# Kernel tuning notes

Measured on AMD Instinct MI355X. Metric: run time of the kernel, lower is better.

The kernel has to match this reference:

```python
import jax, jax.numpy as jnp
import numpy as np

B, N, G, K = 4, 8192, 512, 32          # batch, points, num_group, group_size
D, H, DEPTH, ENC, MLP = 768, 12, 4, 256, 3072
HD = D // H


def _fps(xyz, npoint):
    """Farthest point sampling, starts at index 0 (as pointnet2_utils). xyz: [B,N,3] -> idx [B,npoint]."""
    b, n, _ = xyz.shape
    def step(carry, _):
        dmin, far = carry                                   # dmin [b,n], far [b]
        c = jax.vmap(lambda p, i: p[i])(xyz, far)           # [b,3]
        d = jnp.sum((xyz - c[:, None, :]) ** 2, -1)         # [b,n]
        dmin = jnp.minimum(dmin, d)
        nxt = jnp.argmax(dmin, -1).astype(jnp.int32)
        return (dmin, nxt), far
    init = (jnp.full((b, n), 1e10, jnp.float32), jnp.zeros((b,), jnp.int32))
    _, idx = jax.lax.scan(step, init, None, length=npoint)
    return jnp.transpose(idx)                                # [b, npoint]


def _sqdist(a, b):
    # [B,S,C] x [B,M,C] -> [B,S,M] squared euclidean
    return (jnp.sum(a * a, -1)[:, :, None]
            - 2.0 * jnp.einsum('bsc,bmc->bsm', a, b)
            + jnp.sum(b * b, -1)[:, None, :])


def _bn(x, g, b, m, v):   # eval-mode BatchNorm1d, channels-last
    return (x - m) * jax.lax.rsqrt(v + 1e-5) * g + b


def _ln(x, g, b):
    mu = jnp.mean(x, -1, keepdims=True)
    va = jnp.var(x, -1, keepdims=True)
    return (x - mu) * jax.lax.rsqrt(va + 1e-5) * g + b


def setup_inputs():
    key = jax.random.key(0)
    cnt = [0]
    def rn(shape, s=0.02):
        cnt[0] += 1
        return jax.random.normal(jax.random.fold_in(key, cnt[0]), shape, jnp.float32) * s
    inp = dict(
        pts=jax.random.uniform(jax.random.fold_in(key, 1000), (B, N, 3), jnp.float32),
        colors=jax.random.uniform(jax.random.fold_in(key, 1001), (B, N, 3), jnp.float32),
        enc_w1a=rn((128, 6), 0.2), enc_b1a=rn((128,)),
        bn1_g=jnp.ones((128,)), bn1_b=jnp.zeros((128,)), bn1_m=jnp.zeros((128,)), bn1_v=jnp.ones((128,)),
        enc_w1b=rn((256, 128), 0.05), enc_b1b=rn((256,)),
        enc_w2a=rn((512, 512), 0.03), enc_b2a=rn((512,)),
        bn2_g=jnp.ones((512,)), bn2_b=jnp.zeros((512,)), bn2_m=jnp.zeros((512,)), bn2_v=jnp.ones((512,)),
        enc_w2b=rn((ENC, 512), 0.03), enc_b2b=rn((ENC,)),
        e2t_w=rn((D, ENC), 0.04), e2t_b=rn((D,)),
        cls_token=jnp.zeros((1, 1, D)), cls_pos=rn((1, 1, D), 1.0),
        pe_w1=rn((128, 3), 0.3), pe_b1=rn((128,)),
        pe_w2=rn((D, 128), 0.05), pe_b2=rn((D,)),
        ln1_g=jnp.ones((DEPTH, D)), ln1_b=jnp.zeros((DEPTH, D)),
        qkv_w=rn((DEPTH, D, 3 * D)), qkv_b=rn((DEPTH, 3 * D)),
        proj_w=rn((DEPTH, D, D)), proj_b=rn((DEPTH, D)),
        ln2_g=jnp.ones((DEPTH, D)), ln2_b=jnp.zeros((DEPTH, D)),
        mlp_w1=rn((DEPTH, D, MLP)), mlp_b1=rn((DEPTH, MLP)),
        mlp_w2=rn((DEPTH, MLP, D)), mlp_b2=rn((DEPTH, D)),
        fcn_g=jnp.ones((D,)), fcn_b=jnp.zeros((D,)),
        t2e_w=rn((D, D)), t2e_b=rn((D,)),
    )
    return inp


def reference(pts, colors, enc_w1a, enc_b1a, bn1_g, bn1_b, bn1_m, bn1_v,
              enc_w1b, enc_b1b, enc_w2a, enc_b2a, bn2_g, bn2_b, bn2_m, bn2_v,
              enc_w2b, enc_b2b, e2t_w, e2t_b, cls_token, cls_pos,
              pe_w1, pe_b1, pe_w2, pe_b2,
              ln1_g, ln1_b, qkv_w, qkv_b, proj_w, proj_b,
              ln2_g, ln2_b, mlp_w1, mlp_b1, mlp_w2, mlp_b2,
              fcn_g, fcn_b, t2e_w, t2e_b):
    b = pts.shape[0]
    # ---- Group: FPS centers + kNN grouping ----
    fidx = _fps(pts, G)                                        # [B,G]
    center = jax.vmap(lambda p, i: p[i])(pts, fidx)            # [B,G,3]
    d = _sqdist(center, pts)                                   # [B,G,N]
    _, knn = jax.lax.top_k(-d, K)                              # [B,G,K] smallest dists
    nbr = jax.vmap(lambda p, i: p[i])(pts, knn)                # [B,G,K,3]
    nbr_c = jax.vmap(lambda p, i: p[i])(colors, knn)           # [B,G,K,3]
    nbr = nbr - center[:, :, None, :]
    feat = jnp.concatenate([nbr, nbr_c], -1)                   # [B,G,K,6]
    # ---- mini-PointNet Encoder (conv1d k=1 == linear over channels) ----
    x = feat.reshape(b * G, K, 6)
    f = jax.nn.relu(_bn(x @ enc_w1a.T + enc_b1a, bn1_g, bn1_b, bn1_m, bn1_v))
    f = f @ enc_w1b.T + enc_b1b                                # [M,K,256]
    fg = jnp.max(f, axis=1, keepdims=True)                     # [M,1,256]
    f = jnp.concatenate([jnp.broadcast_to(fg, (b * G, K, 256)), f], -1)  # [M,K,512]
    f = jax.nn.relu(_bn(f @ enc_w2a.T + enc_b2a, bn2_g, bn2_b, bn2_m, bn2_v))
    f = f @ enc_w2b.T + enc_b2b                                # [M,K,ENC]
    tok = jnp.max(f, axis=1).reshape(b, G, ENC)                # [B,G,ENC]
    # ---- to transformer ----
    tok = tok @ e2t_w.T + e2t_b                                # [B,G,D]
    pos = jax.nn.gelu(center @ pe_w1.T + pe_b1, approximate=False) @ pe_w2.T + pe_b2
    xs = jnp.concatenate([jnp.broadcast_to(cls_token, (b, 1, D)), tok], 1)
    ps = jnp.concatenate([jnp.broadcast_to(cls_pos, (b, 1, D)), pos], 1)
    xs = xs + ps                                               # [B,G+1,D]
    s = G + 1
    scale = HD ** -0.5
    for i in range(DEPTH):
        h = _ln(xs, ln1_g[i], ln1_b[i])
        qkv = (h @ qkv_w[i] + qkv_b[i]).reshape(b, s, 3, H, HD)
        q, k, v = qkv[:, :, 0], qkv[:, :, 1], qkv[:, :, 2]
        att = jax.nn.softmax(jnp.einsum('bshd,bthd->bhst', q, k) * scale, -1)
        o = jnp.einsum('bhst,bthd->bshd', att, v).reshape(b, s, D)
        xs = xs + o @ proj_w[i] + proj_b[i]
        h = _ln(xs, ln2_g[i], ln2_b[i])
        h = jax.nn.gelu(h @ mlp_w1[i] + mlp_b1[i], approximate=False) @ mlp_w2[i] + mlp_b2[i]
        xs = xs + h
    xs = _ln(xs, fcn_g, fcn_b)
    return xs @ t2e_w.T + t2e_b                                # [B,G+1,embed_dim]
```

## Files before the change

### kernel.cpp

```cpp
#include <hip/hip_runtime.h>
#include <math.h>

#define BB 4
#define NN 8192
#define GG 512
#define KK 32
#define DD 768
#define SS 513
#define HH 12

typedef __attribute__((ext_vector_type(8))) short bf16x8;
typedef __attribute__((ext_vector_type(4))) float f32x4;

__device__ __forceinline__ float gelu_f(float x) {
  return 0.5f * x * (1.f + erff(x * 0.70710678118654752f));
}
__device__ __forceinline__ unsigned short f2b(float f) {
  unsigned u = __float_as_uint(f);
  u = (u + 0x7FFFu + ((u >> 16) & 1u)) >> 16;
  return (unsigned short)u;
}
__device__ __forceinline__ float b2f(unsigned short h) {
  return __uint_as_float(((unsigned)h) << 16);
}

__device__ __forceinline__ unsigned wave_max_u32(unsigned v) {
  unsigned t;
  t = (unsigned)__builtin_amdgcn_update_dpp(0, (int)v, 0x111, 0xf, 0xf, false); v = t > v ? t : v;
  t = (unsigned)__builtin_amdgcn_update_dpp(0, (int)v, 0x112, 0xf, 0xf, false); v = t > v ? t : v;
  t = (unsigned)__builtin_amdgcn_update_dpp(0, (int)v, 0x114, 0xf, 0xf, false); v = t > v ? t : v;
  t = (unsigned)__builtin_amdgcn_update_dpp(0, (int)v, 0x118, 0xf, 0xf, false); v = t > v ? t : v;
  t = (unsigned)__builtin_amdgcn_update_dpp(0, (int)v, 0x142, 0xf, 0xf, false); v = t > v ? t : v;
  t = (unsigned)__builtin_amdgcn_update_dpp(0, (int)v, 0x143, 0xf, 0xf, false); v = t > v ? t : v;
  return (unsigned)__builtin_amdgcn_readlane((int)v, 63);
}
__device__ __forceinline__ unsigned wave_min_u32(unsigned v) {
  unsigned t;
  t = (unsigned)__builtin_amdgcn_update_dpp(0x7FFFFFFF, (int)v, 0x111, 0xf, 0xf, false); v = t < v ? t : v;
  t = (unsigned)__builtin_amdgcn_update_dpp(0x7FFFFFFF, (int)v, 0x112, 0xf, 0xf, false); v = t < v ? t : v;
  t = (unsigned)__builtin_amdgcn_update_dpp(0x7FFFFFFF, (int)v, 0x114, 0xf, 0xf, false); v = t < v ? t : v;
  t = (unsigned)__builtin_amdgcn_update_dpp(0x7FFFFFFF, (int)v, 0x118, 0xf, 0xf, false); v = t < v ? t : v;
  t = (unsigned)__builtin_amdgcn_update_dpp(0x7FFFFFFF, (int)v, 0x142, 0xf, 0xf, false); v = t < v ? t : v;
  t = (unsigned)__builtin_amdgcn_update_dpp(0x7FFFFFFF, (int)v, 0x143, 0xf, 0xf, false); v = t < v ? t : v;
  return (unsigned)__builtin_amdgcn_readlane((int)v, 63);
}

__global__ __launch_bounds__(512) void fps_kernel(const float* __restrict__ pts,
                                                  int* __restrict__ fidx,
                                                  float* __restrict__ center) {
  int b = blockIdx.x;
  int tid = threadIdx.x;
  const float* P = pts + (size_t)b * NN * 3;
  float x[16], y[16], z[16], dmin[16];
#pragma unroll
  for (int j = 0; j < 16; j++) {
    int p = tid + 512 * j;
    x[j] = P[p * 3 + 0]; y[j] = P[p * 3 + 1]; z[j] = P[p * 3 + 2];
    dmin[j] = 1e10f;
  }
  __shared__ unsigned long long sbest;
  __shared__ float scx, scy, scz;
  if (tid == 0) {
    sbest = 0ull;
    scx = x[0]; scy = y[0]; scz = z[0];
    fidx[b * GG] = 0;
    center[(size_t)(b * GG) * 3 + 0] = x[0];
    center[(size_t)(b * GG) * 3 + 1] = y[0];
    center[(size_t)(b * GG) * 3 + 2] = z[0];
  }
  __syncthreads();
  for (int it = 0; it < GG - 1; it++) {
    float cx = scx, cy = scy, cz = scz;
    unsigned bv = 0u, bi = 0x7FFFFFFFu;
    int bj = 0;
#pragma unroll
    for (int j = 0; j < 16; j++) {
      float dx = __fsub_rn(x[j], cx);
      float dy = __fsub_rn(y[j], cy);
      float dz = __fsub_rn(z[j], cz);
      float d = __fadd_rn(__fadd_rn(__fmul_rn(dx, dx), __fmul_rn(dy, dy)), __fmul_rn(dz, dz));
      float dm = fminf(dmin[j], d);
      dmin[j] = dm;
      unsigned db = __float_as_uint(dm);
      if (db > bv) { bv = db; bi = (unsigned)(tid + 512 * j); bj = j; }
    }
    unsigned wmax = wave_max_u32(bv);
    unsigned cand = (bv == wmax) ? bi : 0x7FFFFFFFu;
    unsigned widx = wave_min_u32(cand);
    bool wave_winner = (bv == wmax) && (bi == widx);
    unsigned long long mykey = ((unsigned long long)wmax << 32) | (unsigned long long)(0xFFFFFFFFu - widx);
    if (wave_winner) atomicMax(&sbest, mykey);
    __syncthreads();
    if (wave_winner) {
      if (sbest == mykey) {
        scx = x[bj]; scy = y[bj]; scz = z[bj];
        fidx[b * GG + it + 1] = (int)bi;
        center[(size_t)(b * GG + it + 1) * 3 + 0] = x[bj];
        center[(size_t)(b * GG + it + 1) * 3 + 1] = y[bj];
        center[(size_t)(b * GG + it + 1) * 3 + 2] = z[bj];
        sbest = 0ull;
      }
    }
    __syncthreads();
  }
}

__global__ __launch_bounds__(256) void knn_kernel(const float* __restrict__ pts,
                                                  const float* __restrict__ center,
                                                  int* __restrict__ knn_idx) {
  int bg = blockIdx.x;
  int b = bg >> 9;
  int tid = threadIdx.x;
  __shared__ float dist[NN];
  __shared__ unsigned long long sred[4];
  const float* P = pts + (size_t)b * NN * 3;
  float cx = center[bg * 3 + 0], cy = center[bg * 3 + 1], cz = center[bg * 3 + 2];
  for (int j = 0; j < 32; j++) {
    int p = tid + 256 * j;
    float dx = P[p * 3 + 0] - cx, dy = P[p * 3 + 1] - cy, dz = P[p * 3 + 2] - cz;
    dist[p] = dx * dx + dy * dy + dz * dz;
  }
  __syncthreads();
  for (int r = 0; r < KK; r++) {
    unsigned long long best = 0xFFFFFFFFFFFFFFFFull;
#pragma unroll 8
    for (int j = 0; j < 32; j++) {
      int p = tid + 256 * j;
      unsigned long long key = ((unsigned long long)__float_as_uint(dist[p]) << 32) | (unsigned)p;
      best = (key < best) ? key : best;
    }
#pragma unroll
    for (int off = 32; off > 0; off >>= 1) {
      unsigned long long o = __shfl_xor(best, off);
      best = (o < best) ? o : best;
    }
    int lane = tid & 63, wid = tid >> 6;
    if (lane == 0) sred[wid] = best;
    __syncthreads();
    if (tid < 4) {
      unsigned long long v = sred[tid];
      unsigned long long o = __shfl_xor(v, 1); v = (o < v) ? o : v;
      o = __shfl_xor(v, 2); v = (o < v) ? o : v;
      if (tid == 0) {
        int p = (int)(v & 0xFFFFFFFFu);
        knn_idx[bg * KK + r] = p;
        dist[p] = 3.0e38f;
      }
    }
    __syncthreads();
  }
}

__global__ __launch_bounds__(256) void cvt_kernel(const float* __restrict__ s,
                                                  unsigned short* __restrict__ d, int n) {
  int i = (blockIdx.x * 256 + threadIdx.x) * 4;
  if (i + 3 < n) {
    float4 v = *reinterpret_cast<const float4*>(&s[i]);
    d[i + 0] = f2b(v.x); d[i + 1] = f2b(v.y); d[i + 2] = f2b(v.z); d[i + 3] = f2b(v.w);
  }
}

__global__ __launch_bounds__(256) void tc_kernel(const float* __restrict__ src,
                                                 unsigned short* __restrict__ dst,
                                                 int K, int N) {
  __shared__ float t[32][33];
  int n0 = blockIdx.x * 32, k0 = blockIdx.y * 32;
  int tx = threadIdx.x & 31, ty = threadIdx.x >> 5;
#pragma unroll
  for (int i = 0; i < 32; i += 8)
    t[ty + i][tx] = src[(size_t)(k0 + ty + i) * N + n0 + tx];
  __syncthreads();
#pragma unroll
  for (int i = 0; i < 32; i += 8)
    dst[(size_t)(n0 + ty + i) * K + k0 + tx] = f2b(t[tx][ty + i]);
}

__global__ __launch_bounds__(256) void enc1a_kernel(
    const float* __restrict__ pts, const float* __restrict__ colors,
    const int* __restrict__ knn_idx, const float* __restrict__ center,
    const float* __restrict__ w1a, const float* __restrict__ b1a,
    const float* __restrict__ bn1g, const float* __restrict__ bn1b,
    const float* __restrict__ bn1m, const float* __restrict__ bn1v,
    unsigned short* __restrict__ f1, int gbase)
{
  int g = gbase + blockIdx.x;
  int b = g >> 9;
  int tid = threadIdx.x;
  __shared__ float feat[KK][8];
  if (tid < 192) {
    int k = tid / 6, c = tid % 6;
    int p = knn_idx[g * KK + k];
    float v;
    if (c < 3) v = pts[(size_t)(b * NN + p) * 3 + c] - center[g * 3 + c];
    else       v = colors[(size_t)(b * NN + p) * 3 + (c - 3)];
    feat[k][c] = v;
  }
  __syncthreads();
  for (int e = tid; e < KK * 128; e += 256) {
    int k = e >> 7, j = e & 127;
    float s = b1a[j];
#pragma unroll
    for (int c = 0; c < 6; c++) s += feat[k][c] * w1a[j * 6 + c];
    s = (s - bn1m[j]) * rsqrtf(bn1v[j] + 1e-5f) * bn1g[j] + bn1b[j];
    f1[((size_t)blockIdx.x * KK + k) * 128 + j] = f2b(fmaxf(s, 0.f));
  }
}

__global__ __launch_bounds__(256) void maxpool_kernel(const unsigned short* __restrict__ in,
                                                      unsigned short* __restrict__ out, int total) {
  int e = blockIdx.x * 256 + threadIdx.x;
  if (e >= total) return;
  int g = e >> 8, c = e & 255;
  const unsigned short* p = in + ((size_t)g * 32) * 256 + c;
  float m = -3e38f;
#pragma unroll 8
  for (int k = 0; k < 32; k++) m = fmaxf(m, b2f(p[k * 256]));
  out[e] = f2b(m);
}

template <int ACT, int RESID, int OUTBF, int CONCAT>
__global__ __launch_bounds__(256) void bgemm(
    const unsigned short* __restrict__ A, const unsigned short* __restrict__ fg,
    const unsigned short* __restrict__ W, const float* __restrict__ bias,
    const float* __restrict__ resid, void* __restrict__ outp,
    int M, int N, int K,
    const float* __restrict__ bng, const float* __restrict__ bnb,
    const float* __restrict__ bnm, const float* __restrict__ bnv)
{
  __shared__ unsigned short As[128][40];
  __shared__ unsigned short Bs[128][40];
  const int tid = threadIdx.x;
  const int tm0 = blockIdx.y * 128, tn0 = blockIdx.x * 128;
  const int w = tid >> 6, l = tid & 63;
  const int wr = (w >> 1) * 64, wc = (w & 1) * 64;
  const int lr = l & 15, lk = l >> 4;

  f32x4 zero4 = {0.f, 0.f, 0.f, 0.f};
  f32x4 acc[4][4];
#pragma unroll
  for (int m = 0; m < 4; m++)
#pragma unroll
    for (int n = 0; n < 4; n++) acc[m][n] = zero4;

  for (int k0 = 0; k0 < K; k0 += 32) {
#pragma unroll
    for (int c = 0; c < 2; c++) {
      int s = tid + c * 256;
      int row = s >> 2, kp = s & 3;
      uint4 va = make_uint4(0u, 0u, 0u, 0u);
      int grow = tm0 + row;
      if (grow < M) {
        if (CONCAT) {
          int kk = k0 + kp * 8;
          const unsigned short* src = (kk < 256)
              ? &fg[((size_t)(grow >> 5)) * 256 + kk]
              : &A[(size_t)grow * 256 + (kk - 256)];
          va = *reinterpret_cast<const uint4*>(src);
        } else {
          va = *reinterpret_cast<const uint4*>(&A[(size_t)grow * K + k0 + kp * 8]);
        }
      }
      *reinterpret_cast<uint4*>(&As[row][kp * 8]) = va;
      uint4 vb = *reinterpret_cast<const uint4*>(&W[(size_t)(tn0 + row) * K + k0 + kp * 8]);
      *reinterpret_cast<uint4*>(&Bs[row][kp * 8]) = vb;
    }
    __syncthreads();
    bf16x8 af[4], bfr[4];
#pragma unroll
    for (int m = 0; m < 4; m++)
      af[m] = *reinterpret_cast<const bf16x8*>(&As[wr + m * 16 + lr][lk * 8]);
#pragma unroll
    for (int n = 0; n < 4; n++)
      bfr[n] = *reinterpret_cast<const bf16x8*>(&Bs[wc + n * 16 + lr][lk * 8]);
#pragma unroll
    for (int m = 0; m < 4; m++)
#pragma unroll
      for (int n = 0; n < 4; n++)
        acc[m][n] = __builtin_amdgcn_mfma_f32_16x16x32_bf16(af[m], bfr[n], acc[m][n], 0, 0, 0);
    __syncthreads();
  }
#pragma unroll
  for (int m = 0; m < 4; m++) {
#pragma unroll
    for (int r = 0; r < 4; r++) {
      int row = tm0 + wr + m * 16 + lk * 4 + r;
      if (row >= M) continue;
#pragma unroll
      for (int n = 0; n < 4; n++) {
        int col = tn0 + wc + n * 16 + lr;
        float v = acc[m][n][r] + bias[col];
        if (ACT == 1) v = gelu_f(v);
        if (ACT == 2) {
          v = (v - bnm[col]) * rsqrtf(bnv[col] + 1e-5f) * bng[col] + bnb[col];
          v = fmaxf(v, 0.f);
        }
        if (RESID) v += resid[(size_t)row * N + col];
        if (OUTBF) ((unsigned short*)outp)[(size_t)row * N + col] = f2b(v);
        else       ((float*)outp)[(size_t)row * N + col] = v;
      }
    }
  }
}

template <int TRANSB, int ACT, int RESID>
__global__ __launch_bounds__(256) void gemm_kernel(
    const float* __restrict__ A, const float* __restrict__ W,
    const float* __restrict__ bias, const float* __restrict__ resid,
    float* __restrict__ out, int M, int N, int K)
{
  __shared__ float Asm[16][64];
  __shared__ float Bsm[16][64];
  int tile_n = blockIdx.x * 64, tile_m = blockIdx.y * 64;
  int tid = threadIdx.x;
  int tm = tid >> 4, tn = tid & 15;
  float acc[4][4] = {};
  for (int k0 = 0; k0 < K; k0 += 16) {
    {
      int e = tid * 4;
      int m = e >> 4, k = e & 15;
      int row = tile_m + m;
      float4 v = make_float4(0.f, 0.f, 0.f, 0.f);
      if (row < M) v = *reinterpret_cast<const float4*>(&A[(size_t)row * K + k0 + k]);
      Asm[k + 0][m] = v.x; Asm[k + 1][m] = v.y; Asm[k + 2][m] = v.z; Asm[k + 3][m] = v.w;
    }
    if (TRANSB == 0) {
      int e = tid * 4;
      int n = e & 63, k = e >> 6;
      float4 v = *reinterpret_cast<const float4*>(&W[(size_t)(k0 + k) * N + tile_n + n]);
      *reinterpret_cast<float4*>(&Bsm[k][n]) = v;
    } else {
      int e = tid * 4;
      int k = e & 15, n = e >> 4;
      float4 v = *reinterpret_cast<const float4*>(&W[(size_t)(tile_n + n) * K + k0 + k]);
      Bsm[k + 0][n] = v.x; Bsm[k + 1][n] = v.y; Bsm[k + 2][n] = v.z; Bsm[k + 3][n] = v.w;
    }
    __syncthreads();
#pragma unroll
    for (int kk = 0; kk < 16; kk++) {
      float4 a = *reinterpret_cast<const float4*>(&Asm[kk][tm * 4]);
      float4 wv = *reinterpret_cast<const float4*>(&Bsm[kk][tn * 4]);
      acc[0][0] += a.x * wv.x; acc[0][1] += a.x * wv.y; acc[0][2] += a.x * wv.z; acc[0][3] += a.x * wv.w;
      acc[1][0] += a.y * wv.x; acc[1][1] += a.y * wv.y; acc[1][2] += a.y * wv.z; acc[1][3] += a.y * wv.w;
      acc[2][0] += a.z * wv.x; acc[2][1] += a.z * wv.y; acc[2][2] += a.z * wv.z; acc[2][3] += a.z * wv.w;
      acc[3][0] += a.w * wv.x; acc[3][1] += a.w * wv.y; acc[3][2] += a.w * wv.z; acc[3][3] += a.w * wv.w;
    }
    __syncthreads();
  }
#pragma unroll
  for (int i = 0; i < 4; i++) {
    int row = tile_m + tm * 4 + i;
    if (row >= M) continue;
    int col = tile_n + tn * 4;
    float4 r;
    r.x = acc[i][0] + bias[col + 0];
    r.y = acc[i][1] + bias[col + 1];
    r.z = acc[i][2] + bias[col + 2];
    r.w = acc[i][3] + bias[col + 3];
    if (ACT == 1) { r.x = gelu_f(r.x); r.y = gelu_f(r.y); r.z = gelu_f(r.z); r.w = gelu_f(r.w); }
    if (RESID) {
      float4 rr = *reinterpret_cast<const float4*>(&resid[(size_t)row * N + col]);
      r.x += rr.x; r.y += rr.y; r.z += rr.z; r.w += rr.w;
    }
    *reinterpret_cast<float4*>(&out[(size_t)row * N + col]) = r;
  }
}

template <int OUTBF>
__global__ __launch_bounds__(256) void ln_kernel(const float* __restrict__ x,
                                                 const float* __restrict__ g,
                                                 const float* __restrict__ bta,
                                                 void* __restrict__ yv) {
  int r = blockIdx.x;
  int tid = threadIdx.x;
  __shared__ float sred[4];
  __shared__ float smu, srs;
  const float* xr = x + (size_t)r * 768;
  float v0 = xr[tid], v1 = xr[tid + 256], v2 = xr[tid + 512];
  float s = v0 + v1 + v2;
#pragma unroll
  for (int off = 32; off > 0; off >>= 1) s += __shfl_xor(s, off);
  if ((tid & 63) == 0) sred[tid >> 6] = s;
  __syncthreads();
  if (tid < 4) {
    float t = sred[tid];
    t += __shfl_xor(t, 1); t += __shfl_xor(t, 2);
    if (tid == 0) smu = t * (1.f / 768.f);
  }
  __syncthreads();
  float mu = smu;
  float d0 = v0 - mu, d1 = v1 - mu, d2 = v2 - mu;
  float ss = d0 * d0 + d1 * d1 + d2 * d2;
#pragma unroll
  for (int off = 32; off > 0; off >>= 1) ss += __shfl_xor(ss, off);
  if ((tid & 63) == 0) sred[tid >> 6] = ss;
  __syncthreads();
  if (tid < 4) {
    float t = sred[tid];
    t += __shfl_xor(t, 1); t += __shfl_xor(t, 2);
    if (tid == 0) srs = rsqrtf(t * (1.f / 768.f) + 1e-5f);
  }
  __syncthreads();
  float rs = srs;
  float o0 = d0 * rs * g[tid]       + bta[tid];
  float o1 = d1 * rs * g[tid + 256] + bta[tid + 256];
  float o2 = d2 * rs * g[tid + 512] + bta[tid + 512];
  if (OUTBF) {
    unsigned short* yr = (unsigned short*)yv + (size_t)r * 768;
    yr[tid] = f2b(o0); yr[tid + 256] = f2b(o1); yr[tid + 512] = f2b(o2);
  } else {
    float* yr = (float*)yv + (size_t)r * 768;
    yr[tid] = o0; yr[tid + 256] = o1; yr[tid + 512] = o2;
  }
}

__global__ __launch_bounds__(256) void pe_hidden_kernel(const float* __restrict__ center,
                                                        const float* __restrict__ w1,
                                                        const float* __restrict__ b1,
                                                        float* __restrict__ hid) {
  int e = blockIdx.x * 256 + threadIdx.x;
  int r = e >> 7, j = e & 127;
  float cx = center[r * 3 + 0], cy = center[r * 3 + 1], cz = center[r * 3 + 2];
  float s = b1[j] + cx * w1[j * 3 + 0] + cy * w1[j * 3 + 1] + cz * w1[j * 3 + 2];
  hid[e] = gelu_f(s);
}

__global__ __launch_bounds__(256) void assemble_kernel(const float* __restrict__ tp,
                                                       const float* __restrict__ pp,
                                                       const float* __restrict__ cls_tok,
                                                       const float* __restrict__ cls_pos,
                                                       float* __restrict__ xs) {
  int r = blockIdx.x;
  int b = r / SS, t = r % SS;
  int tid = threadIdx.x;
  float* xr = xs + (size_t)r * 768;
  if (t == 0) {
    for (int d = tid; d < 768; d += 256) xr[d] = cls_tok[d] + cls_pos[d];
  } else {
    int g = b * GG + (t - 1);
    for (int d = tid; d < 768; d += 256) xr[d] = tp[(size_t)g * 768 + d] + pp[(size_t)g * 768 + d];
  }
}

__global__ __launch_bounds__(256) void flash_kernel(const float* __restrict__ qkv,
                                                    unsigned short* __restrict__ o) {
  int qt = blockIdx.x, h = blockIdx.y, b = blockIdx.z;
  int tid = threadIdx.x;
  int rr = tid >> 2, cg = tid & 3;
  __shared__ float Ks[64][68];
  __shared__ float Vs[64][68];
  __shared__ float Ps[64][68];
  const float scale = 0.125f;
  int qrow = qt * 64 + rr;
  bool qvalid = qrow < SS;
  float q[64];
  {
    const float* qp = qkv + (size_t)(b * SS + (qvalid ? qrow : 0)) * 2304 + h * 64;
#pragma unroll
    for (int i = 0; i < 64; i += 4) {
      float4 v = *reinterpret_cast<const float4*>(qp + i);
      q[i + 0] = qvalid ? v.x * scale : 0.f;
      q[i + 1] = qvalid ? v.y * scale : 0.f;
      q[i + 2] = qvalid ? v.z * scale : 0.f;
      q[i + 3] = qvalid ? v.w * scale : 0.f;
    }
  }
  float O[16];
#pragma unroll
  for (int i = 0; i < 16; i++) O[i] = 0.f;
  float mrow = -3e38f, lrow = 0.f;
  for (int kc = 0; kc < 9; kc++) {
    int kbase = kc * 64;
#pragma unroll
    for (int e = tid; e < 1024; e += 256) {
      int krow = e >> 4, d0 = (e & 15) * 4;
      int gk = kbase + krow;
      float4 kv = make_float4(0.f, 0.f, 0.f, 0.f);
      float4 vv = make_float4(0.f, 0.f, 0.f, 0.f);
      if (gk < SS) {
        const float* pk = qkv + (size_t)(b * SS + gk) * 2304 + 768 + h * 64 + d0;
        kv = *reinterpret_cast<const float4*>(pk);
        vv = *reinterpret_cast<const float4*>(pk + 768);
      }
      *reinterpret_cast<float4*>(&Ks[krow][d0]) = kv;
      *reinterpret_cast<float4*>(&Vs[krow][d0]) = vv;
    }
    __syncthreads();
    float svals[16];
    float mc = -3e38f;
#pragma unroll 4
    for (int jj = 0; jj < 16; jj++) {
      int kk = jj * 4 + cg;
      const float* kr = &Ks[kk][0];
      float p0 = 0.f, p1 = 0.f, p2 = 0.f, p3 = 0.f;
#pragma unroll
      for (int i = 0; i < 64; i += 4) {
        float4 kv4 = *reinterpret_cast<const float4*>(kr + i);
        p0 += q[i + 0] * kv4.x; p1 += q[i + 1] * kv4.y;
        p2 += q[i + 2] * kv4.z; p3 += q[i + 3] * kv4.w;
      }
      float p = (p0 + p1) + (p2 + p3);
      float s = (kbase + kk < SS) ? p : -3e38f;
      svals[jj] = s;
      mc = fmaxf(mc, s);
    }
    mc = fmaxf(mc, __shfl_xor(mc, 1));
    mc = fmaxf(mc, __shfl_xor(mc, 2));
    float mnew = fmaxf(mrow, mc);
    float alpha = __expf(mrow - mnew);
    float lsum = 0.f;
#pragma unroll
    for (int jj = 0; jj < 16; jj++) {
      float pexp = __expf(svals[jj] - mnew);
      lsum += pexp;
      Ps[rr][jj * 4 + cg] = pexp;
    }
    lsum += __shfl_xor(lsum, 1);
    lsum += __shfl_xor(lsum, 2);
    lrow = lrow * alpha + lsum;
#pragma unroll
    for (int i = 0; i < 16; i++) O[i] *= alpha;
    mrow = mnew;
#pragma unroll 4
    for (int kk = 0; kk < 64; kk++) {
      float pw = Ps[rr][kk];
      const float* vr = &Vs[kk][cg * 16];
#pragma unroll
      for (int i = 0; i < 16; i++) O[i] += pw * vr[i];
    }
    __syncthreads();
  }
  if (qvalid) {
    float inv = 1.f / lrow;
    unsigned short* op = o + (size_t)(b * SS + qrow) * 768 + h * 64 + cg * 16;
#pragma unroll
    for (int i = 0; i < 16; i++) op[i] = f2b(O[i] * inv);
  }
}

extern "C" void kernel_launch(void* const* d_in, const int* in_sizes, int n_in,
                              void* d_out, int out_size, void* d_ws, size_t ws_size,
                              hipStream_t stream) {
  const float* pts    = (const float*)d_in[0];
  const float* colors = (const float*)d_in[1];
  const float* w1a    = (const float*)d_in[2];
  const float* b1a    = (const float*)d_in[3];
  const float* bn1g   = (const float*)d_in[4];
  const float* bn1b   = (const float*)d_in[5];
  const float* bn1m   = (const float*)d_in[6];
  const float* bn1v   = (const float*)d_in[7];
  const float* w1b    = (const float*)d_in[8];
  const float* b1b    = (const float*)d_in[9];
  const float* w2a    = (const float*)d_in[10];
  const float* b2a    = (const float*)d_in[11];
  const float* bn2g   = (const float*)d_in[12];
  const float* bn2b   = (const float*)d_in[13];
  const float* bn2m   = (const float*)d_in[14];
  const float* bn2v   = (const float*)d_in[15];
  const float* w2b    = (const float*)d_in[16];
  const float* b2b    = (const float*)d_in[17];
  const float* e2t_w  = (const float*)d_in[18];
  const float* e2t_b  = (const float*)d_in[19];
  const float* cls_token = (const float*)d_in[20];
  const float* cls_pos   = (const float*)d_in[21];
  const float* pe_w1  = (const float*)d_in[22];
  const float* pe_b1  = (const float*)d_in[23];
  const float* pe_w2  = (const float*)d_in[24];
  const float* pe_b2  = (const float*)d_in[25];
  const float* ln1_g  = (const float*)d_in[26];
  const float* ln1_b  = (const float*)d_in[27];
  const float* qkv_w  = (const float*)d_in[28];
  const float* qkv_b  = (const float*)d_in[29];
  const float* proj_w = (const float*)d_in[30];
  const float* proj_b = (const float*)d_in[31];
  const float* ln2_g  = (const float*)d_in[32];
  const float* ln2_b  = (const float*)d_in[33];
  const float* mlp_w1 = (const float*)d_in[34];
  const float* mlp_b1 = (const float*)d_in[35];
  const float* mlp_w2 = (const float*)d_in[36];
  const float* mlp_b2 = (const float*)d_in[37];
  const float* fcn_g  = (const float*)d_in[38];
  const float* fcn_b  = (const float*)d_in[39];
  const float* t2e_w  = (const float*)d_in[40];
  const float* t2e_b  = (const float*)d_in[41];

  if (ws_size < (size_t)67174400) return;

  char* ws = (char*)d_ws;
  int*            fidx   = (int*)(ws + 0);
  float*          center = (float*)(ws + 8192);
  int*            knn    = (int*)(ws + 32768);
  unsigned short* tok    = (unsigned short*)(ws + 294912);
  float*          xs     = (float*)(ws + 1343488);
  unsigned short* hbuf   = (unsigned short*)(ws + 7647232);
  float*          fbuf   = (float*)(ws + 10799104);
  char*           WT     = ws + 17102848;
  unsigned short* qkv_wt = (unsigned short*)(WT + 0);
  unsigned short* proj_wt= (unsigned short*)(WT + 3538944);
  unsigned short* w1t    = (unsigned short*)(WT + 4718592);
  unsigned short* w2t    = (unsigned short*)(WT + 9437184);
  unsigned short* w1bb   = (unsigned short*)(WT + 14155776);
  unsigned short* w2ab   = (unsigned short*)(WT + 14221312);
  unsigned short* w2bb   = (unsigned short*)(WT + 14745600);
  unsigned short* e2tb   = (unsigned short*)(WT + 15007744);
  char*           BA     = ws + 32503808;
  unsigned short* f1   = (unsigned short*)(BA + 0);
  unsigned short* f2   = (unsigned short*)(BA + 4194304);
  unsigned short* fg   = (unsigned short*)(BA + 12582912);
  unsigned short* f3   = (unsigned short*)(BA + 12845056);
  unsigned short* f4   = (unsigned short*)(BA + 0);
  float*          tp   = (float*)(BA + 0);
  float*          pp   = (float*)(BA + 6291456);
  float*          hid  = (float*)(BA + 12582912);
  float*          qkvb = (float*)(BA + 0);
  unsigned short* obuf = (unsigned short*)(BA + 18911232);
  unsigned short* mh   = (unsigned short*)(BA + 22063104);

  cvt_kernel<<<32, 256, 0, stream>>>(w1b, w1bb, 32768);
  cvt_kernel<<<256, 256, 0, stream>>>(w2a, w2ab, 262144);
  cvt_kernel<<<128, 256, 0, stream>>>(w2b, w2bb, 131072);
  cvt_kernel<<<192, 256, 0, stream>>>(e2t_w, e2tb, 196608);

  fps_kernel<<<BB, 512, 0, stream>>>(pts, fidx, center);
  knn_kernel<<<BB * GG, 256, 0, stream>>>(pts, center, knn);

  for (int c = 0; c < 4; c++) {
    int gbase = c * 512;
    enc1a_kernel<<<512, 256, 0, stream>>>(pts, colors, knn, center,
        w1a, b1a, bn1g, bn1b, bn1m, bn1v, f1, gbase);
    bgemm<0, 0, 1, 0><<<dim3(2, 128), 256, 0, stream>>>(f1, nullptr, w1bb, b1b,
        nullptr, f2, 16384, 256, 128, nullptr, nullptr, nullptr, nullptr);
    maxpool_kernel<<<512, 256, 0, stream>>>(f2, fg, 512 * 256);
    bgemm<2, 0, 1, 1><<<dim3(4, 128), 256, 0, stream>>>(f2, fg, w2ab, b2a,
        nullptr, f3, 16384, 512, 512, bn2g, bn2b, bn2m, bn2v);
    bgemm<0, 0, 1, 0><<<dim3(2, 128), 256, 0, stream>>>(f3, nullptr, w2bb, b2b,
        nullptr, f4, 16384, 256, 512, nullptr, nullptr, nullptr, nullptr);
    maxpool_kernel<<<512, 256, 0, stream>>>(f4, tok + (size_t)gbase * 256, 512 * 256);
  }

  bgemm<0, 0, 0, 0><<<dim3(6, 16), 256, 0, stream>>>(tok, nullptr, e2tb, e2t_b,
      nullptr, tp, 2048, 768, 256, nullptr, nullptr, nullptr, nullptr);
  pe_hidden_kernel<<<1024, 256, 0, stream>>>(center, pe_w1, pe_b1, hid);
  gemm_kernel<1, 0, 0><<<dim3(12, 32), 256, 0, stream>>>(hid, pe_w2, pe_b2, nullptr, pp, 2048, 768, 128);
  assemble_kernel<<<BB * SS, 256, 0, stream>>>(tp, pp, cls_token, cls_pos, xs);

  for (int i = 0; i < 4; i++) {
    tc_kernel<<<dim3(72, 24), 256, 0, stream>>>(qkv_w + (size_t)i * 768 * 2304, qkv_wt, 768, 2304);
    tc_kernel<<<dim3(24, 24), 256, 0, stream>>>(proj_w + (size_t)i * 768 * 768, proj_wt, 768, 768);
    tc_kernel<<<dim3(96, 24), 256, 0, stream>>>(mlp_w1 + (size_t)i * 768 * 3072, w1t, 768, 3072);
    tc_kernel<<<dim3(24, 96), 256, 0, stream>>>(mlp_w2 + (size_t)i * 3072 * 768, w2t, 3072, 768);

    ln_kernel<1><<<BB * SS, 256, 0, stream>>>(xs, ln1_g + i * 768, ln1_b + i * 768, hbuf);
    bgemm<0, 0, 0, 0><<<dim3(18, 17), 256, 0, stream>>>(hbuf, nullptr, qkv_wt,
        qkv_b + i * 2304, nullptr, qkvb, 2052, 2304, 768, nullptr, nullptr, nullptr, nullptr);
    flash_kernel<<<dim3(9, 12, 4), 256, 0, stream>>>(qkvb, obuf);
    bgemm<0, 1, 0, 0><<<dim3(6, 17), 256, 0, stream>>>(obuf, nullptr, proj_wt,
        proj_b + i * 768, xs, xs, 2052, 768, 768, nullptr, nullptr, nullptr, nullptr);
    ln_kernel<1><<<BB * SS, 256, 0, stream>>>(xs, ln2_g + i * 768, ln2_b + i * 768, hbuf);
    bgemm<1, 0, 1, 0><<<dim3(24, 17), 256, 0, stream>>>(hbuf, nullptr, w1t,
        mlp_b1 + i * 3072, nullptr, mh, 2052, 3072, 768, nullptr, nullptr, nullptr, nullptr);
    bgemm<0, 1, 0, 0><<<dim3(6, 17), 256, 0, stream>>>(mh, nullptr, w2t,
        mlp_b2 + i * 768, xs, xs, 2052, 768, 3072, nullptr, nullptr, nullptr, nullptr);
  }

  ln_kernel<0><<<BB * SS, 256, 0, stream>>>(xs, fcn_g, fcn_b, fbuf);
  gemm_kernel<1, 0, 0><<<dim3(12, 33), 256, 0, stream>>>(fbuf, t2e_w, t2e_b, nullptr,
      (float*)d_out, 2052, 768, 768);
}
```

Measured before the change: 2.736 ms.

## Restructure FPS loop with packed math and single-barrier wave reduction

Rewrites the farthest-point-sampling kernel to keep the point cloud in shared memory, use packed v_pk_add/v_pk_mul float2 arithmetic over contiguous per-thread points, and replace the atomicMax plus two-barrier selection with per-wave keys in a double-buffered shared array reduced redundantly by every thread after one barrier. The aim is to cut per-iteration synchronisation and ALU cost in this serial 511-step loop. Points become contiguous per thread instead of strided, which changes the global load pattern and adds 96KB of LDS. The distance is now computed as x+(-c), which is numerically the same as subtraction, and ties still resolve to the lowest index.

```diff
diff --git a/kernel.cpp b/kernel.cpp
--- a/kernel.cpp
+++ b/kernel.cpp
@@ -11,6 +11,7 @@
 
 typedef __attribute__((ext_vector_type(8))) short bf16x8;
 typedef __attribute__((ext_vector_type(4))) float f32x4;
+typedef __attribute__((ext_vector_type(2))) float f32x2;
 
 __device__ __forceinline__ float gelu_f(float x) {
   return 0.5f * x * (1.f + erff(x * 0.70710678118654752f));
@@ -22,6 +23,17 @@
 }
 __device__ __forceinline__ float b2f(unsigned short h) {
   return __uint_as_float(((unsigned)h) << 16);
+}
+
+__device__ __forceinline__ f32x2 pk_add(f32x2 a, f32x2 b) {
+  f32x2 r;
+  asm("v_pk_add_f32 %0, %1, %2" : "=v"(r) : "v"(a), "v"(b));
+  return r;
+}
+__device__ __forceinline__ f32x2 pk_mul(f32x2 a, f32x2 b) {
+  f32x2 r;
+  asm("v_pk_mul_f32 %0, %1, %2" : "=v"(r) : "v"(a), "v"(b));
+  return r;
 }
 
 __device__ __forceinline__ unsigned wave_max_u32(unsigned v) {
@@ -48,60 +60,80 @@
 __global__ __launch_bounds__(512) void fps_kernel(const float* __restrict__ pts,
                                                   int* __restrict__ fidx,
                                                   float* __restrict__ center) {
-  int b = blockIdx.x;
-  int tid = threadIdx.x;
+  int b = blockIdx.x, tid = threadIdx.x;
   const float* P = pts + (size_t)b * NN * 3;
-  float x[16], y[16], z[16], dmin[16];
-#pragma unroll
-  for (int j = 0; j < 16; j++) {
-    int p = tid + 512 * j;
-    x[j] = P[p * 3 + 0]; y[j] = P[p * 3 + 1]; z[j] = P[p * 3 + 2];
-    dmin[j] = 1e10f;
-  }
-  __shared__ unsigned long long sbest;
-  __shared__ float scx, scy, scz;
+  __shared__ float pl[NN * 3];
+  __shared__ unsigned long long skey[2][8];
+  f32x2 x2[8], y2[8], z2[8], dmin2[8];
+  int base = tid * 16;
+#pragma unroll
+  for (int m = 0; m < 8; m++) {
+    const float* p0 = P + (size_t)(base + 2 * m) * 3;
+    float a0 = p0[0], a1 = p0[1], a2 = p0[2], a3 = p0[3], a4 = p0[4], a5 = p0[5];
+    x2[m].x = a0; x2[m].y = a3;
+    y2[m].x = a1; y2[m].y = a4;
+    z2[m].x = a2; z2[m].y = a5;
+    dmin2[m].x = 1e10f; dmin2[m].y = 1e10f;
+    float* q = &pl[(base + 2 * m) * 3];
+    q[0] = a0; q[1] = a1; q[2] = a2; q[3] = a3; q[4] = a4; q[5] = a5;
+  }
+  __syncthreads();
   if (tid == 0) {
-    sbest = 0ull;
-    scx = x[0]; scy = y[0]; scz = z[0];
     fidx[b * GG] = 0;
-    center[(size_t)(b * GG) * 3 + 0] = x[0];
-    center[(size_t)(b * GG) * 3 + 1] = y[0];
-    center[(size_t)(b * GG) * 3 + 2] = z[0];
-  }
-  __syncthreads();
+    center[(size_t)(b * GG) * 3 + 0] = pl[0];
+    center[(size_t)(b * GG) * 3 + 1] = pl[1];
+    center[(size_t)(b * GG) * 3 + 2] = pl[2];
+  }
+  unsigned widx = 0;
   for (int it = 0; it < GG - 1; it++) {
-    float cx = scx, cy = scy, cz = scz;
-    unsigned bv = 0u, bi = 0x7FFFFFFFu;
-    int bj = 0;
-#pragma unroll
-    for (int j = 0; j < 16; j++) {
-      float dx = __fsub_rn(x[j], cx);
-      float dy = __fsub_rn(y[j], cy);
-      float dz = __fsub_rn(z[j], cz);
-      float d = __fadd_rn(__fadd_rn(__fmul_rn(dx, dx), __fmul_rn(dy, dy)), __fmul_rn(dz, dz));
-      float dm = fminf(dmin[j], d);
-      dmin[j] = dm;
-      unsigned db = __float_as_uint(dm);
-      if (db > bv) { bv = db; bi = (unsigned)(tid + 512 * j); bj = j; }
-    }
-    unsigned wmax = wave_max_u32(bv);
-    unsigned cand = (bv == wmax) ? bi : 0x7FFFFFFFu;
-    unsigned widx = wave_min_u32(cand);
-    bool wave_winner = (bv == wmax) && (bi == widx);
-    unsigned long long mykey = ((unsigned long long)wmax << 32) | (unsigned long long)(0xFFFFFFFFu - widx);
-    if (wave_winner) atomicMax(&sbest, mykey);
-    __syncthreads();
-    if (wave_winner) {
-      if (sbest == mykey) {
-        scx = x[bj]; scy = y[bj]; scz = z[bj];
-        fidx[b * GG + it + 1] = (int)bi;
-        center[(size_t)(b * GG + it + 1) * 3 + 0] = x[bj];
-        center[(size_t)(b * GG + it + 1) * 3 + 1] = y[bj];
-        center[(size_t)(b * GG + it + 1) * 3 + 2] = z[bj];
-        sbest = 0ull;
-      }
-    }
-    __syncthreads();
+    float cx = pl[widx * 3 + 0], cy = pl[widx * 3 + 1], cz = pl[widx * 3 + 2];
+    f32x2 ncx, ncy, ncz;
+    ncx.x = -cx; ncx.y = -cx;
+    ncy.x = -cy; ncy.y = -cy;
+    ncz.x = -cz; ncz.y = -cz;
+    float bv = -1.f;
+#pragma unroll
+    for (int m = 0; m < 8; m++) {
+      f32x2 dx = pk_add(x2[m], ncx);
+      f32x2 dy = pk_add(y2[m], ncy);
+      f32x2 dz = pk_add(z2[m], ncz);
+      f32x2 xx = pk_mul(dx, dx);
+      f32x2 yy = pk_mul(dy, dy);
+      f32x2 zz = pk_mul(dz, dz);
+      f32x2 d  = pk_add(pk_add(xx, yy), zz);
+      f32x2 dm;
+      dm.x = fminf(dmin2[m].x, d.x);
+      dm.y = fminf(dmin2[m].y, d.y);
+      dmin2[m] = dm;
+      bv = fmaxf(bv, fmaxf(dm.x, dm.y));
+    }
+    unsigned bi = 0xFFFFFFFFu;
+#pragma unroll
+    for (int m = 7; m >= 0; m--) {
+      if (dmin2[m].y == bv) bi = (unsigned)(base + 2 * m + 1);
+      if (dmin2[m].x == bv) bi = (unsigned)(base + 2 * m);
+    }
+    unsigned bvb = __float_as_uint(bv);
+    unsigned wmax = wave_max_u32(bvb);
+    unsigned cand = (bvb == wmax) ? bi : 0xFFFFFFFFu;
+    unsigned wi = wave_min_u32(cand);
+    if ((tid & 63) == 0)
+      skey[it & 1][tid >> 6] =
+          ((unsigned long long)wmax << 32) | (unsigned long long)(0xFFFFFFFFu - wi);
+    __syncthreads();
+    unsigned long long bk = skey[it & 1][0];
+#pragma unroll
+    for (int ww = 1; ww < 8; ww++) {
+      unsigned long long k = skey[it & 1][ww];
+      bk = (k > bk) ? k : bk;
+    }
+    widx = 0xFFFFFFFFu - (unsigned)(bk & 0xFFFFFFFFu);
+    if (tid == 0) {
+      fidx[b * GG + it + 1] = (int)widx;
+      center[(size_t)(b * GG + it + 1) * 3 + 0] = pl[widx * 3 + 0];
+      center[(size_t)(b * GG + it + 1) * 3 + 1] = pl[widx * 3 + 1];
+      center[(size_t)(b * GG + it + 1) * 3 + 2] = pl[widx * 3 + 2];
+    }
   }
 }
 
```

Result: no change. 2.689 ms (-1.7%).
